# Performance work log

Measured on AMD Instinct MI355X. Metric: run time of the kernel, lower is better.

Reference implementation:

```python
import jax, jax.numpy as jnp
import numpy as np

H = 2048      # num_hidden
B = 2048      # batch_size
T = 64        # seq_length
C = 10        # num_classes


def setup_inputs() -> dict:
    key = jax.random.key(0)
    k = jax.random.split(key, 4)
    bound = float(np.sqrt(1.0 / H))  # uniform(-bound, bound) init as in the torch module
    return {
        "x": jax.random.normal(k[0], (B, T), dtype=jnp.float32),
        "W_hx": jax.random.uniform(k[1], (H, 1), jnp.float32, -bound, bound),
        "W_hh": jax.random.uniform(k[2], (H, H), jnp.float32, -bound, bound),
        "W_hy": jax.random.uniform(k[3], (H, C), jnp.float32, -bound, bound),
        "b_h": jnp.zeros((H, 1), jnp.float32),
        "b_p": jnp.zeros((C, 1), jnp.float32),
    }


def reference(x, W_hx, W_hh, W_hy, b_h, b_p):
    # x: [B, T]; hidden state kept as [H, B] to match the torch layout.
    xT = x.T  # [T, B] so scan iterates over time

    def step(h, xt):
        # W_hx @ x_t  : [H,1] @ [1,B] -> [H,B]; W_hh @ h : [H,B]
        h = jnp.tanh(W_hx @ xt[None, :] + W_hh @ h + b_h)
        return h, None

    h0 = jnp.zeros((W_hh.shape[0], x.shape[0]), x.dtype)
    hT, _ = jax.lax.scan(step, h0, xT)
    out = W_hy.T @ hT + b_p  # [C, B]
    return out.T             # [B, C]
```

## Files before the change

### kernel.cpp

```cpp
#include <hip/hip_runtime.h>
#include <cstdint>
#include <cstddef>
#include <cmath>

#define H  2048
#define BB 2048
#define TT 64
#define NC 10

typedef __bf16 bf16;
typedef bf16  bf16x8 __attribute__((ext_vector_type(8)));
typedef float f32x4  __attribute__((ext_vector_type(4)));

__device__ __forceinline__ void load_lds16(const void* g, void* l) {
    __builtin_amdgcn_global_load_lds(
        (__attribute__((address_space(1))) void*)(void*)g,
        (__attribute__((address_space(3))) void*)l,
        16, 0, 0);
}

__global__ void w_shuffle_kernel(const float* __restrict__ Whh,
                                 bf16* __restrict__ Wshuf) {
    int tid = blockIdx.x * blockDim.x + threadIdx.x;
    int sub = tid >> 6;
    int l   = tid & 63;
    int n16 = sub >> 6;
    int k32 = sub & 63;
    int n = n16 * 16 + (l & 15);
    int k = k32 * 32 + (l >> 4) * 8;
    const float* src = Whh + (size_t)n * H + k;
    bf16x8 o;
#pragma unroll
    for (int j = 0; j < 8; ++j) o[j] = (bf16)src[j];
    *(bf16x8*)(Wshuf + (size_t)tid * 8) = o;
}

__global__ void rnn_init(const float* __restrict__ x,
                         const float* __restrict__ Whx,
                         const float* __restrict__ bh,
                         bf16* __restrict__ S) {
    int b  = blockIdx.x;
    int i0 = threadIdx.x * 8;
    float xv = x[(size_t)b * TT];
    bf16x8 o;
#pragma unroll
    for (int j = 0; j < 8; ++j)
        o[j] = (bf16)tanhf(Whx[i0 + j] * xv + bh[i0 + j]);
    size_t sub  = (size_t)(b >> 4) * 64 + (i0 >> 5);
    size_t slot = (size_t)(b & 15) | (size_t)(((i0 >> 3) & 3) << 4);
    *(bf16x8*)(S + (sub * 64 + slot) * 8) = o;
}

#define PH_WAIT(NSTR) asm volatile("s_waitcnt vmcnt(" NSTR ")" ::: "memory")
#define SBAR0()       __builtin_amdgcn_sched_barrier(0)

__launch_bounds__(512, 2)
__global__ void rnn_step(const float* __restrict__ x,
                         const float* __restrict__ Whx,
                         const float* __restrict__ bh,
                         const bf16*  __restrict__ Wshuf,
                         const bf16*  __restrict__ Sr,
                         bf16* __restrict__ Sw,
                         int t) {
    __shared__ __align__(16) char Ls[4][32768];

    const int tid  = threadIdx.x;
    const int w    = tid >> 6;
    const int lane = tid & 63;
    const int lrow = lane & 15;
    const int quad = lane >> 4;

    const int xcd = blockIdx.x & 7;
    const int loc = blockIdx.x >> 3;
    const int bm0 = (loc >> 1) * 128;
    const int bn0 = xcd * 256 + (loc & 1) * 128;

    const int kh   = w >> 2;
    const int s    = w & 3;
    const int qm   = s & 1;
    const int qn   = s >> 1;
    const int cn0  = bn0 + qn * 64;
    const int kh16 = kh * 16;

    const char* srcA = (const char*)Sr +
        ((size_t)((bm0 >> 4) + w) * 64) * 1024 + (size_t)lane * 16;
    const char* srcB = (const char*)Wshuf +
        ((size_t)((bn0 >> 4) + w) * 64) * 1024 + (size_t)lane * 16;

    f32x4 acc[4][4];
#pragma unroll
    for (int i = 0; i < 4; ++i)
#pragma unroll
        for (int j = 0; j < 4; ++j) acc[i][j] = (f32x4){0.f, 0.f, 0.f, 0.f};

    bf16x8 Ae[4], Be[4], Ao[4], Bo[4];

#define ISSUE(RI, pp)                                                        \
    {                                                                        \
        load_lds16(srcA + (size_t)(pp) * 1024,        &Ls[RI][w * 1024]);    \
        load_lds16(srcB + (size_t)(pp) * 1024,        &Ls[RI][(8 + w) * 1024]); \
        load_lds16(srcA + (size_t)(32 + (pp)) * 1024, &Ls[RI][(16 + w) * 1024]); \
        load_lds16(srcB + (size_t)(32 + (pp)) * 1024, &Ls[RI][(24 + w) * 1024]); \
    }

#define DSREAD(Ax, Bx, RI)                                                   \
    {                                                                        \
        _Pragma("unroll")                                                    \
        for (int fm = 0; fm < 4; ++fm)                                       \
            Ax[fm] = *(const bf16x8*)&Ls[RI]                                 \
                [(kh16 + qm * 4 + fm) * 1024 + lane * 16];                   \
        _Pragma("unroll")                                                    \
        for (int fn = 0; fn < 4; ++fn)                                       \
            Bx[fn] = *(const bf16x8*)&Ls[RI]                                 \
                [(kh16 + 8 + qn * 4 + fn) * 1024 + lane * 16];               \
    }

#define MFMAS(Ax, Bx)                                                        \
    {                                                                        \
        __builtin_amdgcn_s_setprio(1);                                       \
        _Pragma("unroll")                                                    \
        for (int fm = 0; fm < 4; ++fm)                                       \
            _Pragma("unroll")                                                \
            for (int fn = 0; fn < 4; ++fn)                                   \
                acc[fm][fn] = __builtin_amdgcn_mfma_f32_16x16x32_bf16(       \
                    Ax[fm], Bx[fn], acc[fm][fn], 0, 0, 0);                   \
        __builtin_amdgcn_s_setprio(0);                                       \
    }

#define PHASE(RNext, RIss, p, W, DOISS, DOREAD, AN, BN, AC, BC)              \
    {                                                                        \
        PH_WAIT(W);                                                          \
        SBAR0();                                                             \
        __builtin_amdgcn_s_barrier();                                        \
        SBAR0();                                                             \
        if (DOISS) ISSUE(RIss, (p) + 3);                                     \
        if (DOREAD) DSREAD(AN, BN, RNext);                                   \
        MFMAS(AC, BC);                                                       \
    }

    ISSUE(0, 0); SBAR0();
    ISSUE(1, 1); SBAR0();
    ISSUE(2, 2); SBAR0();
    PH_WAIT("8");
    SBAR0();
    __builtin_amdgcn_s_barrier();
    SBAR0();
    DSREAD(Ae, Be, 0);

#pragma unroll 1
    for (int q = 0; q < 7; ++q) {
        int p = 4 * q;
        PHASE(1, 3, p + 0, "4", 1, 1, Ao, Bo, Ae, Be);
        PHASE(2, 0, p + 1, "4", 1, 1, Ae, Be, Ao, Bo);
        PHASE(3, 1, p + 2, "4", 1, 1, Ao, Bo, Ae, Be);
        PHASE(0, 2, p + 3, "4", 1, 1, Ae, Be, Ao, Bo);
    }
    PHASE(1, 3, 28, "4", 1, 1, Ao, Bo, Ae, Be);
    PHASE(2, 0, 29, "4", 0, 1, Ae, Be, Ao, Bo);
    PHASE(3, 1, 30, "0", 0, 1, Ao, Bo, Ae, Be);
    PHASE(0, 2, 31, "0", 0, 0, Ae, Be, Ao, Bo);

#undef PHASE
#undef MFMAS
#undef DSREAD
#undef ISSUE

    char* red = &Ls[0][0];
    const int pairbase = s * 16384;
    if (kh == 0) {
#pragma unroll
        for (int fml = 0; fml < 2; ++fml)
#pragma unroll
            for (int fn = 0; fn < 4; ++fn)
                *(f32x4*)&red[pairbase + (fml * 4 + fn) * 1024 + lane * 16] =
                    acc[2 + fml][fn];
    } else {
#pragma unroll
        for (int fml = 0; fml < 2; ++fml)
#pragma unroll
            for (int fn = 0; fn < 4; ++fn)
                *(f32x4*)&red[pairbase + 8192 + (fml * 4 + fn) * 1024 +
                              lane * 16] = acc[fml][fn];
    }
    __syncthreads();
    f32x4 own[2][4];
    if (kh == 0) {
#pragma unroll
        for (int fml = 0; fml < 2; ++fml)
#pragma unroll
            for (int fn = 0; fn < 4; ++fn)
                own[fml][fn] = acc[fml][fn] + *(const f32x4*)&red[pairbase +
                    8192 + (fml * 4 + fn) * 1024 + lane * 16];
    } else {
#pragma unroll
        for (int fml = 0; fml < 2; ++fml)
#pragma unroll
            for (int fn = 0; fn < 4; ++fn)
                own[fml][fn] = acc[2 + fml][fn] + *(const f32x4*)&red[pairbase +
                    (fml * 4 + fn) * 1024 + lane * 16];
    }

    bf16* Lw = (bf16*)&Ls[2][0] + (size_t)w * 2048;
#pragma unroll
    for (int fml = 0; fml < 2; ++fml) {
        int rb = bm0 + qm * 64 + (kh * 2 + fml) * 16 + quad * 4;
        float xv[4];
#pragma unroll
        for (int r = 0; r < 4; ++r) xv[r] = x[(size_t)(rb + r) * TT + t];
#pragma unroll
        for (int fn = 0; fn < 4; ++fn) {
            int col = cn0 + fn * 16 + lrow;
            float wx = Whx[col], bb = bh[col];
            int cbyte = (fn * 16 + lrow) * 2;
#pragma unroll
            for (int r = 0; r < 4; ++r) {
                int row_l = fml * 16 + quad * 4 + r;
                float z = own[fml][fn][r] + wx * xv[r] + bb;
                *(bf16*)((char*)Lw + row_l * 128 +
                         (cbyte ^ ((row_l & 7) << 4))) = (bf16)tanhf(z);
            }
        }
    }
#pragma unroll
    for (int fml = 0; fml < 2; ++fml) {
#pragma unroll
        for (int kc = 0; kc < 2; ++kc) {
            int row_l = fml * 16 + lrow;
            int cb    = (kc * 64 + quad * 16) ^ ((row_l & 7) << 4);
            bf16x8 v = *(const bf16x8*)((const char*)Lw + row_l * 128 + cb);
            size_t sub = (size_t)((bm0 >> 4) + qm * 4 + kh * 2 + fml) * 64 +
                         (cn0 >> 5) + kc;
            *(bf16x8*)(Sw + (sub * 64 + lane) * 8) = v;
        }
    }
}

__global__ void out_proj(const bf16* __restrict__ S,
                         const float* __restrict__ Why,
                         const float* __restrict__ bp,
                         float* __restrict__ out) {
    int b = blockIdx.x, tid = threadIdx.x;
    int h0 = tid * 8;
    size_t sub  = (size_t)(b >> 4) * 64 + (h0 >> 5);
    size_t slot = (size_t)(b & 15) | (size_t)(((h0 >> 3) & 3) << 4);
    bf16x8 v = *(const bf16x8*)(S + (sub * 64 + slot) * 8);
    float p[NC];
#pragma unroll
    for (int c = 0; c < NC; ++c) p[c] = 0.f;
#pragma unroll
    for (int j = 0; j < 8; ++j) {
        float s = (float)v[j];
        const float* wr = Why + (size_t)(h0 + j) * NC;
#pragma unroll
        for (int c = 0; c < NC; ++c) p[c] += s * wr[c];
    }
    __shared__ float red[256 * NC];
#pragma unroll
    for (int c = 0; c < NC; ++c) red[tid * NC + c] = p[c];
    __syncthreads();
    for (int s = 128; s > 0; s >>= 1) {
        if (tid < s)
#pragma unroll
            for (int c = 0; c < NC; ++c) red[tid * NC + c] += red[(tid + s) * NC + c];
        __syncthreads();
    }
    if (tid < NC) out[(size_t)b * NC + tid] = red[tid] + bp[tid];
}

extern "C" void kernel_launch(void* const* d_in, const int* in_sizes, int n_in,
                              void* d_out, int out_size, void* d_ws, size_t ws_size,
                              hipStream_t stream) {
    const float* x   = (const float*)d_in[0];
    const float* Whx = (const float*)d_in[1];
    const float* Whh = (const float*)d_in[2];
    const float* Why = (const float*)d_in[3];
    const float* bh  = (const float*)d_in[4];
    const float* bp  = (const float*)d_in[5];
    float* out = (float*)d_out;

    bf16* Wshuf = (bf16*)d_ws;
    bf16* S0 = (bf16*)((char*)d_ws + (size_t)8 * 1024 * 1024);
    bf16* S1 = (bf16*)((char*)d_ws + (size_t)16 * 1024 * 1024);

    hipLaunchKernelGGL(w_shuffle_kernel, dim3((H * H / 8) / 256), dim3(256),
                       0, stream, Whh, Wshuf);

    hipLaunchKernelGGL(rnn_init, dim3(BB), dim3(256), 0, stream, x, Whx, bh, S1);

    for (int t = 1; t < TT; ++t) {
        const bf16* Srd = (t & 1) ? S1 : S0;
        bf16*       Swr = (t & 1) ? S0 : S1;
        hipLaunchKernelGGL(rnn_step, dim3(256), dim3(512), 0, stream,
                           x, Whx, bh, Wshuf, Srd, Swr, t);
    }

    hipLaunchKernelGGL(out_proj, dim3(BB), dim3(256), 0, stream, S0, Why, bp, out);
}
```

Baseline: 1.469 ms.

## Load W_hh fragments directly into registers, halving LDS staging per block

The B operand (pre-shuffled W_hh) is no longer staged through LDS with global_load_lds. Each wave now loads its bf16x8 B fragments straight from global memory into registers one phase ahead, while only the A operand (hidden state) is staged in LDS. This halves the shared buffer to 64KB and drops the 2-blocks-per-CU launch bound. It adds an extra __syncthreads before the epilogue reuses LDS, since the reduction region now overlaps the tanh write area. The vmcnt wait counts are retuned to cover the extra in-flight register loads. The cost is redundant per-wave global/L2 traffic for W_hh, which is no longer shared across waves through LDS, plus higher VGPR pressure.

```diff
diff --git a/kernel.cpp b/kernel.cpp
--- a/kernel.cpp
+++ b/kernel.cpp
@@ -54,7 +54,7 @@
 #define PH_WAIT(NSTR) asm volatile("s_waitcnt vmcnt(" NSTR ")" ::: "memory")
 #define SBAR0()       __builtin_amdgcn_sched_barrier(0)
 
-__launch_bounds__(512, 2)
+__launch_bounds__(512)
 __global__ void rnn_step(const float* __restrict__ x,
                          const float* __restrict__ Whx,
                          const float* __restrict__ bh,
@@ -62,7 +62,7 @@
                          const bf16*  __restrict__ Sr,
                          bf16* __restrict__ Sw,
                          int t) {
-    __shared__ __align__(16) char Ls[4][32768];
+    __shared__ __align__(16) char Ls[4][16384];
 
     const int tid  = threadIdx.x;
     const int w    = tid >> 6;
@@ -80,12 +80,11 @@
     const int qm   = s & 1;
     const int qn   = s >> 1;
     const int cn0  = bn0 + qn * 64;
-    const int kh16 = kh * 16;
 
     const char* srcA = (const char*)Sr +
         ((size_t)((bm0 >> 4) + w) * 64) * 1024 + (size_t)lane * 16;
     const char* srcB = (const char*)Wshuf +
-        ((size_t)((bn0 >> 4) + w) * 64) * 1024 + (size_t)lane * 16;
+        ((size_t)(bn0 >> 4) * 64) * 1024 + (size_t)lane * 16;
 
     f32x4 acc[4][4];
 #pragma unroll
@@ -95,24 +94,26 @@
 
     bf16x8 Ae[4], Be[4], Ao[4], Bo[4];
 
-#define ISSUE(RI, pp)                                                        \
+#define ISSUE_A(RI, pp)                                                      \
     {                                                                        \
         load_lds16(srcA + (size_t)(pp) * 1024,        &Ls[RI][w * 1024]);    \
-        load_lds16(srcB + (size_t)(pp) * 1024,        &Ls[RI][(8 + w) * 1024]); \
-        load_lds16(srcA + (size_t)(32 + (pp)) * 1024, &Ls[RI][(16 + w) * 1024]); \
-        load_lds16(srcB + (size_t)(32 + (pp)) * 1024, &Ls[RI][(24 + w) * 1024]); \
-    }
-
-#define DSREAD(Ax, Bx, RI)                                                   \
+        load_lds16(srcA + (size_t)(32 + (pp)) * 1024, &Ls[RI][(8 + w) * 1024]); \
+    }
+
+#define BLOAD(Bx, pp)                                                        \
+    {                                                                        \
+        _Pragma("unroll")                                                    \
+        for (int fn = 0; fn < 4; ++fn)                                       \
+            Bx[fn] = *(const bf16x8*)(srcB +                                 \
+                ((size_t)(qn * 4 + fn) * 64 + 32 * kh + (pp)) * 1024);       \
+    }
+
+#define DSREAD_A(Ax, RI)                                                     \
     {                                                                        \
         _Pragma("unroll")                                                    \
         for (int fm = 0; fm < 4; ++fm)                                       \
             Ax[fm] = *(const bf16x8*)&Ls[RI]                                 \
-                [(kh16 + qm * 4 + fm) * 1024 + lane * 16];                   \
-        _Pragma("unroll")                                                    \
-        for (int fn = 0; fn < 4; ++fn)                                       \
-            Bx[fn] = *(const bf16x8*)&Ls[RI]                                 \
-                [(kh16 + 8 + qn * 4 + fn) * 1024 + lane * 16];               \
+                [(kh * 8 + qm * 4 + fm) * 1024 + lane * 16];                 \
     }
 
 #define MFMAS(Ax, Bx)                                                        \
@@ -133,37 +134,40 @@
         SBAR0();                                                             \
         __builtin_amdgcn_s_barrier();                                        \
         SBAR0();                                                             \
-        if (DOISS) ISSUE(RIss, (p) + 3);                                     \
-        if (DOREAD) DSREAD(AN, BN, RNext);                                   \
+        if (DOISS) ISSUE_A(RIss, (p) + 3);                                   \
+        if (DOREAD) { BLOAD(BN, (p) + 1); DSREAD_A(AN, RNext); }             \
         MFMAS(AC, BC);                                                       \
     }
 
-    ISSUE(0, 0); SBAR0();
-    ISSUE(1, 1); SBAR0();
-    ISSUE(2, 2); SBAR0();
+    ISSUE_A(0, 0); SBAR0();
+    ISSUE_A(1, 1); SBAR0();
+    ISSUE_A(2, 2); SBAR0();
+    BLOAD(Be, 0);  SBAR0();
     PH_WAIT("8");
     SBAR0();
     __builtin_amdgcn_s_barrier();
     SBAR0();
-    DSREAD(Ae, Be, 0);
+    DSREAD_A(Ae, 0);
+
+    PHASE(1, 3, 0, "6", 1, 1, Ao, Bo, Ae, Be);
 
 #pragma unroll 1
     for (int q = 0; q < 7; ++q) {
         int p = 4 * q;
-        PHASE(1, 3, p + 0, "4", 1, 1, Ao, Bo, Ae, Be);
-        PHASE(2, 0, p + 1, "4", 1, 1, Ae, Be, Ao, Bo);
-        PHASE(3, 1, p + 2, "4", 1, 1, Ao, Bo, Ae, Be);
-        PHASE(0, 2, p + 3, "4", 1, 1, Ae, Be, Ao, Bo);
-    }
-    PHASE(1, 3, 28, "4", 1, 1, Ao, Bo, Ae, Be);
-    PHASE(2, 0, 29, "4", 0, 1, Ae, Be, Ao, Bo);
-    PHASE(3, 1, 30, "0", 0, 1, Ao, Bo, Ae, Be);
-    PHASE(0, 2, 31, "0", 0, 0, Ae, Be, Ao, Bo);
+        PHASE(2, 0, p + 1, "10", 1, 1, Ae, Be, Ao, Bo);
+        PHASE(3, 1, p + 2, "10", 1, 1, Ao, Bo, Ae, Be);
+        PHASE(0, 2, p + 3, "10", 1, 1, Ae, Be, Ao, Bo);
+        PHASE(1, 3, p + 4, "10", 1, 1, Ao, Bo, Ae, Be);
+    }
+    PHASE(2, 0, 29, "10", 0, 1, Ae, Be, Ao, Bo);
+    PHASE(3, 1, 30, "8",  0, 1, Ao, Bo, Ae, Be);
+    PHASE(0, 2, 31, "0",  0, 0, Ae, Be, Ao, Bo);
 
 #undef PHASE
 #undef MFMAS
-#undef DSREAD
-#undef ISSUE
+#undef DSREAD_A
+#undef BLOAD
+#undef ISSUE_A
 
     char* red = &Ls[0][0];
     const int pairbase = s * 16384;
@@ -199,8 +203,9 @@
                 own[fml][fn] = acc[2 + fml][fn] + *(const f32x4*)&red[pairbase +
                     (fml * 4 + fn) * 1024 + lane * 16];
     }
-
-    bf16* Lw = (bf16*)&Ls[2][0] + (size_t)w * 2048;
+    __syncthreads();
+
+    bf16* Lw = (bf16*)&Ls[0][0] + (size_t)w * 2048;
 #pragma unroll
     for (int fml = 0; fml < 2; ++fml) {
         int rb = bm0 + qm * 64 + (kh * 2 + fml) * 16 + quad * 4;
```

Measured after the change: 1.730 ms. 17.8% more time.

## Halve workgroup barriers in k-loop by issuing two stages per barrier

Applied to the files above, without the earlier changes.

Restructures the 4-stage LDS pipeline so that only every other phase runs a workgroup barrier, and that phase issues the global-to-LDS loads for two future stages. Odd phases only wait on vmcnt and compute. The per-step x loads are hoisted ahead of the split-K reduction to hide their latency. The tanh staging buffer moves to LDS region 0 behind an extra __syncthreads, since region 2 may now still be in flight. This cuts barrier overhead but deepens the vmcnt waits and adds one sync in the epilogue.

```diff
diff --git a/kernel.cpp b/kernel.cpp
--- a/kernel.cpp
+++ b/kernel.cpp
@@ -127,13 +127,18 @@
         __builtin_amdgcn_s_setprio(0);                                       \
     }
 
-#define PHASE(RNext, RIss, p, W, DOISS, DOREAD, AN, BN, AC, BC)              \
-    {                                                                        \
-        PH_WAIT(W);                                                          \
-        SBAR0();                                                             \
-        __builtin_amdgcn_s_barrier();                                        \
-        SBAR0();                                                             \
-        if (DOISS) ISSUE(RIss, (p) + 3);                                     \
+#define PHASE_E(RNext, RIs1, RIs2, p, W, NISS, DOREAD, AN, BN, AC, BC)       \
+    {                                                                        \
+        SBAR0(); PH_WAIT(W); SBAR0();                                        \
+        __builtin_amdgcn_s_barrier(); SBAR0();                               \
+        if (NISS >= 1) ISSUE(RIs1, (p) + 3);                                 \
+        if (NISS >= 2) ISSUE(RIs2, (p) + 4);                                 \
+        if (DOREAD) DSREAD(AN, BN, RNext);                                   \
+        MFMAS(AC, BC);                                                       \
+    }
+#define PHASE_O(RNext, p, W, DOREAD, AN, BN, AC, BC)                         \
+    {                                                                        \
+        SBAR0(); PH_WAIT(W); SBAR0();                                        \
         if (DOREAD) DSREAD(AN, BN, RNext);                                   \
         MFMAS(AC, BC);                                                       \
     }
@@ -141,29 +146,37 @@
     ISSUE(0, 0); SBAR0();
     ISSUE(1, 1); SBAR0();
     ISSUE(2, 2); SBAR0();
-    PH_WAIT("8");
-    SBAR0();
-    __builtin_amdgcn_s_barrier();
-    SBAR0();
+    PH_WAIT("8"); SBAR0();
+    __builtin_amdgcn_s_barrier(); SBAR0();
     DSREAD(Ae, Be, 0);
 
 #pragma unroll 1
     for (int q = 0; q < 7; ++q) {
         int p = 4 * q;
-        PHASE(1, 3, p + 0, "4", 1, 1, Ao, Bo, Ae, Be);
-        PHASE(2, 0, p + 1, "4", 1, 1, Ae, Be, Ao, Bo);
-        PHASE(3, 1, p + 2, "4", 1, 1, Ao, Bo, Ae, Be);
-        PHASE(0, 2, p + 3, "4", 1, 1, Ae, Be, Ao, Bo);
-    }
-    PHASE(1, 3, 28, "4", 1, 1, Ao, Bo, Ae, Be);
-    PHASE(2, 0, 29, "4", 0, 1, Ae, Be, Ao, Bo);
-    PHASE(3, 1, 30, "0", 0, 1, Ao, Bo, Ae, Be);
-    PHASE(0, 2, 31, "0", 0, 0, Ae, Be, Ao, Bo);
-
-#undef PHASE
+        PHASE_E(1, 3, 0, p + 0, "4", 2, 1, Ao, Bo, Ae, Be);
+        PHASE_O(2,       p + 1, "8",    1, Ae, Be, Ao, Bo);
+        PHASE_E(3, 1, 2, p + 2, "4", 2, 1, Ao, Bo, Ae, Be);
+        PHASE_O(0,       p + 3, "8",    1, Ae, Be, Ao, Bo);
+    }
+    PHASE_E(1, 3, 0, 28, "4", 1, 1, Ao, Bo, Ae, Be);
+    PHASE_O(2,       29, "4",    1, Ae, Be, Ao, Bo);
+    PHASE_E(3, 1, 2, 30, "0", 0, 1, Ao, Bo, Ae, Be);
+    PHASE_O(0,       31, "0",    0, Ae, Be, Ao, Bo);
+
+#undef PHASE_E
+#undef PHASE_O
 #undef MFMAS
 #undef DSREAD
 #undef ISSUE
+
+    float xva[2][4];
+#pragma unroll
+    for (int fml = 0; fml < 2; ++fml) {
+        int rb = bm0 + qm * 64 + (kh * 2 + fml) * 16 + quad * 4;
+#pragma unroll
+        for (int r = 0; r < 4; ++r)
+            xva[fml][r] = x[(size_t)(rb + r) * TT + t];
+    }
 
     char* red = &Ls[0][0];
     const int pairbase = s * 16384;
@@ -199,14 +212,11 @@
                 own[fml][fn] = acc[2 + fml][fn] + *(const f32x4*)&red[pairbase +
                     (fml * 4 + fn) * 1024 + lane * 16];
     }
-
-    bf16* Lw = (bf16*)&Ls[2][0] + (size_t)w * 2048;
+    __syncthreads();
+
+    bf16* Lw = (bf16*)&Ls[0][0] + (size_t)w * 2048;
 #pragma unroll
     for (int fml = 0; fml < 2; ++fml) {
-        int rb = bm0 + qm * 64 + (kh * 2 + fml) * 16 + quad * 4;
-        float xv[4];
-#pragma unroll
-        for (int r = 0; r < 4; ++r) xv[r] = x[(size_t)(rb + r) * TT + t];
 #pragma unroll
         for (int fn = 0; fn < 4; ++fn) {
             int col = cn0 + fn * 16 + lrow;
@@ -215,7 +225,7 @@
 #pragma unroll
             for (int r = 0; r < 4; ++r) {
                 int row_l = fml * 16 + quad * 4 + r;
-                float z = own[fml][fn][r] + wx * xv[r] + bb;
+                float z = own[fml][fn][r] + wx * xva[fml][r] + bb;
                 *(bf16*)((char*)Lw + row_l * 128 +
                          (cbyte ^ ((row_l & 7) << 4))) = (bf16)tanhf(z);
             }
```

Measured after the change: 1.532 ms. 4.3% more time.
